# Kernel optimization log

Hardware: AMD Instinct MI355X
Metric: run time of the kernel (lower is better)

The kernel has to match this reference:

```python
import jax, jax.numpy as jnp
import numpy as np

N = 3072        # num_node
R = 7           # num_relation
ATTN_R = 2      # attn_num_relation
SPACE = R - ATTN_R  # space_information_num = 5
D = 64          # hidden dim
H = 4           # num_heads
DH = D // H     # head dim = 16
WINDOW = 128    # window_size
TOPK = 16       # k
TEMP = 0.5      # temperature
EPS = 1e-5
E = N * 16


def _bn(h):
    # BatchNorm1d (training mode, gamma=1, beta=0): normalize over node axis (-2)
    m = h.mean(axis=-2, keepdims=True)
    v = h.var(axis=-2, keepdims=True)
    return (h - m) / jnp.sqrt(v + EPS)


def setup_inputs() -> dict:
    key = jax.random.key(0)
    ks = jax.random.split(key, 12)
    s = 0.1
    return {
        "x": jax.random.normal(ks[0], (N, D), jnp.float32),
        "edge_weight": jnp.ones((E,), jnp.float32),
        "W_rel_s": jax.random.normal(ks[1], (R, D, D), jnp.float32) * s,
        "W_self_s": jax.random.normal(ks[2], (D, D), jnp.float32) * s,
        "b_s": jnp.zeros((D,), jnp.float32),
        "Wq": jax.random.normal(ks[3], (ATTN_R, D, D), jnp.float32) * s,
        "Wk": jax.random.normal(ks[4], (ATTN_R, D, D), jnp.float32) * s,
        "W_msg": jax.random.normal(ks[5], (R * D, D), jnp.float32) * s,
        "W_self_g": jax.random.normal(ks[6], (D, D), jnp.float32) * s,
        "b_g": jnp.zeros((D,), jnp.float32),
        "node_in": jax.random.randint(ks[7], (E,), 0, N, jnp.int32),
        "node_out": jax.random.randint(ks[8], (E,), 0, N, jnp.int32),
        "relation": jax.random.randint(ks[9], (E,), 0, R, jnp.int32),
    }


def reference(x, edge_weight, W_rel_s, W_self_s, b_s, Wq, Wk, W_msg,
              W_self_g, b_g, node_in, node_out, relation):
    # ---- dense adjacency A[r, i, j] = weight of edge (i -> j, relation r) ----
    # equivalent to sparse_coo(...).to_dense().t().view(N,R,N).permute(1,0,2)
    A = jnp.zeros((R, N, N), x.dtype).at[relation, node_in, node_out].add(edge_weight)

    # ---- relationalGraphStack: per-relation conv -> [R, N, D] ----
    msg = jnp.einsum('rij,id->rjd', A, x)                       # aggregate in-neighbors
    rel_out = jax.nn.relu(_bn(jnp.einsum('rjd,rde->rje', msg, W_rel_s)
                              + x @ W_self_s + b_s))            # [R, N, D]

    # ---- Rewirescorelayer on attention relations ----
    attn_in = rel_out[SPACE:]                                   # [ATTN_R, N, D]
    q = jnp.einsum('rnd,rde->rne', attn_in, Wq).reshape(ATTN_R, N, H, DH)
    kk = jnp.einsum('rnd,rde->rne', attn_in, Wk).reshape(ATTN_R, N, H, DH)
    scores = jnp.einsum('rnhd,rmhd->rhnm', q, kk) / np.sqrt(DH).astype(np.float32)
    idx = jnp.arange(N)
    wmask = jnp.abs(idx[:, None] - idx[None, :]) <= WINDOW      # local window
    scores = jnp.where(wmask[None, None], scores, -1e9)
    probs = jax.nn.softmax(scores / TEMP, axis=-1).mean(axis=1)  # [ATTN_R, N, N]
    kth = jax.lax.top_k(probs, TOPK)[0][..., -1:]
    S = jnp.where(probs >= kth, probs, 0.0)                     # hard top-k per row
    attn_output = jnp.transpose(S, (1, 0, 2)).reshape(N, ATTN_R * N)

    # ---- fuse with adjacency: max over attention blocks, keep spatial blocks ----
    adj2d = jnp.transpose(A, (1, 0, 2)).reshape(N, R * N)       # [i, r*N + j]
    attn_output = jnp.maximum(adj2d[:, SPACE * N:], attn_output)
    new_edge_list = jnp.concatenate([attn_output, adj2d[:, :SPACE * N]], axis=1)

    # ---- rewireGearNetstack: GearNet conv with dense rewired adjacency ----
    B = jnp.transpose(new_edge_list.reshape(N, R, N), (1, 0, 2))  # [R, i, j]
    msg2 = jnp.einsum('rij,id->jrd', B, x).reshape(N, R * D)      # [N, R*D]
    hidden = jax.nn.relu(_bn(msg2 @ W_msg + x @ W_self_g + b_g))  # [N, D]

    graph_feature = hidden.sum(axis=0, keepdims=True)             # SumReadout, 1 graph
    return graph_feature, hidden, new_edge_list
```

## Files before the change

### kernel.cpp

```cpp
#include <hip/hip_runtime.h>
#include <cmath>

constexpr int kN    = 3072;
constexpr int kR    = 7;
constexpr int kSPC  = 5;
constexpr int kD    = 64;
constexpr int kWIN  = 128;
constexpr int kTOPK = 16;
constexpr int kE    = kN * 16;
constexpr int kRN   = kR * kN;
constexpr int kRD   = kR * kD;
constexpr float kEPS = 1e-5f;

__device__ __forceinline__ float wred_max(float v) {
#pragma unroll
  for (int off = 32; off; off >>= 1) v = fmaxf(v, __shfl_xor(v, off));
  return v;
}
__device__ __forceinline__ float wred_sum(float v) {
#pragma unroll
  for (int off = 32; off; off >>= 1) v += __shfl_xor(v, off);
  return v;
}

__global__ __launch_bounds__(256) void k_fill0(float4* __restrict__ p, size_t n4) {
  size_t i = (size_t)blockIdx.x * 256 + threadIdx.x;
  const size_t stride = (size_t)gridDim.x * 256;
  const float4 z = make_float4(0.f, 0.f, 0.f, 0.f);
  for (; i < n4; i += stride) p[i] = z;
}

__global__ __launch_bounds__(256) void k_scatter(
    const float* __restrict__ x, const float* __restrict__ ew,
    const int* __restrict__ nin, const int* __restrict__ nout,
    const int* __restrict__ rel,
    float* __restrict__ msg2, float* __restrict__ msgA, float* __restrict__ nel) {
  const int e = blockIdx.x * 4 + (threadIdx.x >> 6);
  const int lane = threadIdx.x & 63;
  const int r = rel[e], i = nin[e], j = nout[e];
  const float w = ew[e];
  const float v = w * x[i * kD + lane];
  if (r < kSPC) {
    atomicAdd(&msg2[(size_t)j * kRD + (r + 2) * kD + lane], v);
    if (lane == 0) atomicAdd(&nel[(size_t)i * kRN + (size_t)(r + 2) * kN + j], w);
  } else {
    const int k = r - kSPC;
    atomicAdd(&msgA[(size_t)(k * kN + j) * kD + lane], v);
    if (lane == 0) atomicAdd(&nel[(size_t)i * kRN + (size_t)k * kN + j], w);
  }
}

__global__ __launch_bounds__(256) void k_h1(
    const float* __restrict__ x, const float* __restrict__ msgA,
    const float* __restrict__ Wrel, const float* __restrict__ Wself,
    const float* __restrict__ bs, float* __restrict__ h1) {
  const int k = blockIdx.y;
  const int e = threadIdx.x & 63;
  const int rl = threadIdx.x >> 6;
  const int n = blockIdx.x * 4 + rl;
  __shared__ float a[4][kD], xx[4][kD];
  a[rl][e] = msgA[(size_t)(k * kN + n) * kD + e];
  xx[rl][e] = x[n * kD + e];
  __syncthreads();
  const float* Wr = Wrel + (size_t)(kSPC + k) * kD * kD;
  float acc = bs[e];
#pragma unroll 8
  for (int d = 0; d < kD; ++d)
    acc += a[rl][d] * Wr[d * kD + e] + xx[rl][d] * Wself[d * kD + e];
  h1[(size_t)(k * kN + n) * kD + e] = acc;
}

__global__ __launch_bounds__(256) void k_bnstats(
    const float* __restrict__ h, float* __restrict__ mean, float* __restrict__ inv) {
  const int c = blockIdx.x;
  const int mat = c >> 6, e = c & 63;
  const float* p = h + (size_t)mat * kN * kD + e;
  float s = 0.f, s2 = 0.f;
  for (int n = threadIdx.x; n < kN; n += 256) {
    float v = p[(size_t)n * kD];
    s += v; s2 += v * v;
  }
  __shared__ float sh0[256], sh1[256];
  sh0[threadIdx.x] = s; sh1[threadIdx.x] = s2;
  __syncthreads();
  for (int off = 128; off > 0; off >>= 1) {
    if (threadIdx.x < off) { sh0[threadIdx.x] += sh0[threadIdx.x + off]; sh1[threadIdx.x] += sh1[threadIdx.x + off]; }
    __syncthreads();
  }
  if (threadIdx.x == 0) {
    float m = sh0[0] / (float)kN;
    float var = sh1[0] / (float)kN - m * m;
    mean[c] = m;
    inv[c] = rsqrtf(var + kEPS);
  }
}

__global__ __launch_bounds__(256) void k_qk(
    const float* __restrict__ h1, const float* __restrict__ mean,
    const float* __restrict__ inv, const float* __restrict__ Wq,
    const float* __restrict__ Wk, float* __restrict__ qb, float* __restrict__ kb) {
  const int k = blockIdx.y;
  const int e = threadIdx.x & 63;
  const int rl = threadIdx.x >> 6;
  const int n = blockIdx.x * 4 + rl;
  __shared__ float a[4][kD];
  float v = h1[(size_t)(k * kN + n) * kD + e];
  v = (v - mean[k * 64 + e]) * inv[k * 64 + e];
  a[rl][e] = v > 0.f ? v : 0.f;
  __syncthreads();
  const float* wq = Wq + (size_t)k * kD * kD;
  const float* wk = Wk + (size_t)k * kD * kD;
  float aq = 0.f, ak = 0.f;
#pragma unroll 8
  for (int d = 0; d < kD; ++d) {
    float av = a[rl][d];
    aq += av * wq[d * kD + e];
    ak += av * wk[d * kD + e];
  }
  qb[(size_t)(k * kN + n) * kD + e] = aq;
  kb[(size_t)(k * kN + n) * kD + e] = ak;
}

__global__ __launch_bounds__(256) void k_attn(
    const float* __restrict__ qb, const float* __restrict__ kb,
    const float* __restrict__ x, float* __restrict__ nel,
    float* __restrict__ msg2, int* __restrict__ selCols, int* __restrict__ selCnt) {
  const int lane = threadIdx.x & 63;
  const int w = threadIdx.x >> 6;
  const int idx = blockIdx.x * 4 + w;
  const int k = idx / kN;
  const int n = idx - k * kN;
  __shared__ float qs[4][kD];
  __shared__ float sval[4][64];
  __shared__ int scol[4][64];
  qs[w][lane] = qb[(size_t)(k * kN + n) * kD + lane];
  __syncthreads();
  const int lo = n - kWIN < 0 ? 0 : n - kWIN;
  const int hi = n + kWIN > kN - 1 ? kN - 1 : n + kWIN;

  float sc[5][4];
#pragma unroll
  for (int s = 0; s < 5; ++s) {
    const int m = lo + s * 64 + lane;
    if (m <= hi) {
      const float4* krow = reinterpret_cast<const float4*>(kb + (size_t)(k * kN + m) * kD);
#pragma unroll
      for (int h = 0; h < 4; ++h) {
        float acc = 0.f;
#pragma unroll
        for (int g = 0; g < 4; ++g) {
          float4 kv = krow[h * 4 + g];
          const float* qp = &qs[w][h * 16 + g * 4];
          acc += kv.x * qp[0] + kv.y * qp[1] + kv.z * qp[2] + kv.w * qp[3];
        }
        sc[s][h] = acc * 0.5f;
      }
    } else {
#pragma unroll
      for (int h = 0; h < 4; ++h) sc[s][h] = -3.0e38f;
    }
  }

  float pm[5] = {0.f, 0.f, 0.f, 0.f, 0.f};
#pragma unroll
  for (int h = 0; h < 4; ++h) {
    float lm = fmaxf(fmaxf(fmaxf(sc[0][h], sc[1][h]), fmaxf(sc[2][h], sc[3][h])), sc[4][h]);
    float mx = wred_max(lm);
    float eh[5], den = 0.f;
#pragma unroll
    for (int s = 0; s < 5; ++s) {
      eh[s] = (sc[s][h] > -1.0e38f) ? expf(sc[s][h] - mx) : 0.f;
      den += eh[s];
    }
    den = wred_sum(den);
    float rdn = 1.f / den;
#pragma unroll
    for (int s = 0; s < 5; ++s) pm[s] += eh[s] * rdn;
  }
#pragma unroll
  for (int s = 0; s < 5; ++s) pm[s] *= 0.25f;

  float rem[5];
#pragma unroll
  for (int s = 0; s < 5; ++s) {
    const int m = lo + s * 64 + lane;
    rem[s] = (m <= hi) ? pm[s] : -1.f;
  }
  float kth = 0.f;
  for (int t = 0; t < kTOPK; ++t) {
    float lm = fmaxf(fmaxf(fmaxf(rem[0], rem[1]), fmaxf(rem[2], rem[3])), rem[4]);
    float gm = wred_max(lm);
    unsigned long long b = __ballot(lm == gm);
    int src = __ffsll((unsigned long long)b) - 1;
    if (lane == src) {
      if (rem[0] == gm) rem[0] = -2.f;
      else if (rem[1] == gm) rem[1] = -2.f;
      else if (rem[2] == gm) rem[2] = -2.f;
      else if (rem[3] == gm) rem[3] = -2.f;
      else rem[4] = -2.f;
    }
    kth = gm;
  }

  bool sel[5];
  int cl = 0;
#pragma unroll
  for (int s = 0; s < 5; ++s) {
    const int m = lo + s * 64 + lane;
    sel[s] = (m <= hi) && (pm[s] >= kth);
    cl += sel[s] ? 1 : 0;
  }
  int v = cl;
#pragma unroll
  for (int off = 1; off < 64; off <<= 1) {
    int t = __shfl_up(v, off);
    if (lane >= off) v += t;
  }
  const int excl = v - cl;
  const int total = __shfl(v, 63);
  const int tot = total < 64 ? total : 64;
  const int rowbase = (k * kN + n) * 64;
  int p = excl;
#pragma unroll
  for (int s = 0; s < 5; ++s) {
    if (sel[s] && p < 64) {
      const int m = lo + s * 64 + lane;
      const size_t cell = (size_t)n * kRN + (size_t)k * kN + m;
      float a = nel[cell];
      float fin = fmaxf(a, pm[s]);
      nel[cell] = fin;
      scol[w][p] = m;
      sval[w][p] = fin;
      selCols[rowbase + p] = m;
      ++p;
    }
  }
  if (lane == 0) selCnt[k * kN + n] = tot;

  const float xv = x[n * kD + lane];
  for (int t = 0; t < tot; ++t) {
    const int m = scol[w][t];
    const float fv = sval[w][t];
    atomicAdd(&msg2[(size_t)m * kRD + k * kD + lane], fv * xv);
  }
}

__global__ __launch_bounds__(256) void k_edgefix(
    const float* __restrict__ x, const float* __restrict__ ew,
    const int* __restrict__ nin, const int* __restrict__ nout,
    const int* __restrict__ rel, const int* __restrict__ selCols,
    const int* __restrict__ selCnt, float* __restrict__ msg2) {
  const int e = blockIdx.x * 4 + (threadIdx.x >> 6);
  const int lane = threadIdx.x & 63;
  const int r = rel[e];
  if (r < kSPC) return;
  const int k = r - kSPC, i = nin[e], j = nout[e];
  int diff = i - j; if (diff < 0) diff = -diff;
  if (diff <= kWIN) {
    const int cnt = selCnt[k * kN + i];
    bool mine = (lane < cnt) && (selCols[(k * kN + i) * 64 + lane] == j);
    if (__ballot(mine)) return;
  }
  atomicAdd(&msg2[(size_t)j * kRD + k * kD + lane], ew[e] * x[i * kD + lane]);
}

__global__ __launch_bounds__(256) void k_hpre(
    const float* __restrict__ msg2, const float* __restrict__ x,
    const float* __restrict__ Wmsg, const float* __restrict__ Wg,
    const float* __restrict__ bg, float* __restrict__ hpre) {
  const int e = threadIdx.x & 63;
  const int rl = threadIdx.x >> 6;
  const int n0 = blockIdx.x * 4;
  __shared__ float ml[4][kRD];
  __shared__ float xl[4][kD];
  for (int idx = threadIdx.x; idx < 4 * kRD; idx += 256) {
    int rr = idx / kRD, c = idx - rr * kRD;
    ml[rr][c] = msg2[(size_t)(n0 + rr) * kRD + c];
  }
  {
    int rr = threadIdx.x >> 6, c = threadIdx.x & 63;
    xl[rr][c] = x[(n0 + rr) * kD + c];
  }
  __syncthreads();
  float acc = bg[e];
#pragma unroll 8
  for (int c = 0; c < kRD; ++c) acc += ml[rl][c] * Wmsg[c * kD + e];
#pragma unroll 8
  for (int d = 0; d < kD; ++d) acc += xl[rl][d] * Wg[d * kD + e];
  hpre[(size_t)(n0 + rl) * kD + e] = acc;
}

__global__ __launch_bounds__(256) void k_hfin(
    float* __restrict__ hid, const float* __restrict__ mean,
    const float* __restrict__ inv, float* __restrict__ gf) {
  const int e = threadIdx.x & 63;
  const int rl = threadIdx.x >> 6;
  const int n = blockIdx.x * 4 + rl;
  float v = hid[(size_t)n * kD + e];
  v = (v - mean[e]) * inv[e];
  v = v > 0.f ? v : 0.f;
  hid[(size_t)n * kD + e] = v;
  __shared__ float sh[4][kD];
  sh[rl][e] = v;
  __syncthreads();
  if (threadIdx.x < 64)
    atomicAdd(&gf[e], sh[0][e] + sh[1][e] + sh[2][e] + sh[3][e]);
}

extern "C" void kernel_launch(void* const* d_in, const int* in_sizes, int n_in,
                              void* d_out, int out_size, void* d_ws, size_t ws_size,
                              hipStream_t stream) {
  (void)in_sizes; (void)n_in; (void)ws_size;
  const float* x     = (const float*)d_in[0];
  const float* ew    = (const float*)d_in[1];
  const float* Wrel  = (const float*)d_in[2];
  const float* Wself = (const float*)d_in[3];
  const float* bs    = (const float*)d_in[4];
  const float* Wq    = (const float*)d_in[5];
  const float* Wk    = (const float*)d_in[6];
  const float* Wmsg  = (const float*)d_in[7];
  const float* Wg    = (const float*)d_in[8];
  const float* bg    = (const float*)d_in[9];
  const int*   nin   = (const int*)d_in[10];
  const int*   nout  = (const int*)d_in[11];
  const int*   rel   = (const int*)d_in[12];

  float* gf  = (float*)d_out;
  float* hid = gf + 64;
  float* nel = hid + (size_t)kN * kD;

  float* w0    = (float*)d_ws;
  float* msg2  = w0;
  float* msgA  = msg2 + (size_t)kN * kRD;
  float* h1    = msgA + (size_t)2 * kN * kD;
  float* qb    = h1   + (size_t)2 * kN * kD;
  float* kb    = qb   + (size_t)2 * kN * kD;
  float* mean1 = kb   + (size_t)2 * kN * kD;
  float* inv1  = mean1 + 128;
  float* mean2 = inv1 + 128;
  float* inv2  = mean2 + 64;
  int* selCols = (int*)(inv2 + 64);
  int* selCnt  = selCols + (size_t)2 * kN * 64;

  k_fill0<<<2048, 256, 0, stream>>>((float4*)d_out, (size_t)out_size / 4);
  k_fill0<<<512, 256, 0, stream>>>((float4*)msg2,
                                   (size_t)(kN * kRD + 2 * kN * kD) / 4);

  k_scatter<<<kE / 4, 256, 0, stream>>>(x, ew, nin, nout, rel, msg2, msgA, nel);
  dim3 g2(kN / 4, 2);
  k_h1<<<g2, 256, 0, stream>>>(x, msgA, Wrel, Wself, bs, h1);
  k_bnstats<<<128, 256, 0, stream>>>(h1, mean1, inv1);
  k_qk<<<g2, 256, 0, stream>>>(h1, mean1, inv1, Wq, Wk, qb, kb);
  k_attn<<<(2 * kN) / 4, 256, 0, stream>>>(qb, kb, x, nel, msg2, selCols, selCnt);
  k_edgefix<<<kE / 4, 256, 0, stream>>>(x, ew, nin, nout, rel, selCols, selCnt, msg2);
  k_hpre<<<kN / 4, 256, 0, stream>>>(msg2, x, Wmsg, Wg, bg, hid);
  k_bnstats<<<64, 256, 0, stream>>>(hid, mean2, inv2);
  k_hfin<<<kN / 4, 256, 0, stream>>>(hid, mean2, inv2, gf);
}
```

Before: 228.2 us.

## Spread dense edge-list zero-fill across pipeline kernels and write it last

The large dense new_edge_list output (about 264 MB) is no longer zeroed up front in one fill kernel. Its zeroing is split into eight chunks, and each chunk is cleared inside one of the existing compute kernels. Edge weights for the attention relations inside the window now go into a compact windowed buffer that the attention kernel reads. The final dense cells are written at the end by two small scatter kernels, one for the edges and one for the selected top-k values. This is meant to overlap the memory-bound fill with latency-bound compute, at the cost of extra grid-stride loops in every kernel and more workspace.

Measured after the change: 223.8 us. No clear change (-1.9%).

```diff
diff --git a/kernel.cpp b/kernel.cpp
--- a/kernel.cpp
+++ b/kernel.cpp
@@ -10,7 +10,13 @@
 constexpr int kE    = kN * 16;
 constexpr int kRN   = kR * kN;
 constexpr int kRD   = kR * kD;
+constexpr int kAW   = 2 * kWIN + 1;
 constexpr float kEPS = 1e-5f;
+
+constexpr size_t kNelF = (size_t)kN * kRN;
+constexpr size_t kNelQ = kNelF / 4;
+constexpr int    kCar  = 8;
+constexpr size_t kChunkQ = kNelQ / kCar;
 
 __device__ __forceinline__ float wred_max(float v) {
 #pragma unroll
@@ -23,18 +29,31 @@
   return v;
 }
 
-__global__ __launch_bounds__(256) void k_fill0(float4* __restrict__ p, size_t n4) {
+__device__ __forceinline__ void fill_chunk(float4* __restrict__ nel4, int cid) {
+  const size_t beg = (size_t)cid * kChunkQ;
+  const size_t end = beg + kChunkQ;
+  const size_t nth = (size_t)gridDim.x * gridDim.y * blockDim.x;
+  size_t tid = ((size_t)blockIdx.y * gridDim.x + blockIdx.x) * blockDim.x + threadIdx.x;
+  const float4 z = make_float4(0.f, 0.f, 0.f, 0.f);
+  for (size_t i = beg + tid; i < end; i += nth) nel4[i] = z;
+}
+
+__global__ __launch_bounds__(256) void k_fill_ws(float4* __restrict__ p, size_t n4,
+                                                 float* __restrict__ gf) {
   size_t i = (size_t)blockIdx.x * 256 + threadIdx.x;
   const size_t stride = (size_t)gridDim.x * 256;
   const float4 z = make_float4(0.f, 0.f, 0.f, 0.f);
   for (; i < n4; i += stride) p[i] = z;
-}
-
-__global__ __launch_bounds__(256) void k_scatter(
+  if (blockIdx.x == 0 && threadIdx.x < 64) gf[threadIdx.x] = 0.f;
+}
+
+__global__ __launch_bounds__(256) void k_scatter_msg(
     const float* __restrict__ x, const float* __restrict__ ew,
     const int* __restrict__ nin, const int* __restrict__ nout,
-    const int* __restrict__ rel,
-    float* __restrict__ msg2, float* __restrict__ msgA, float* __restrict__ nel) {
+    const int* __restrict__ rel, float* __restrict__ msg2,
+    float* __restrict__ msgA, float* __restrict__ awin,
+    float4* __restrict__ nel4) {
+  fill_chunk(nel4, 0);
   const int e = blockIdx.x * 4 + (threadIdx.x >> 6);
   const int lane = threadIdx.x & 63;
   const int r = rel[e], i = nin[e], j = nout[e];
@@ -42,18 +61,21 @@
   const float v = w * x[i * kD + lane];
   if (r < kSPC) {
     atomicAdd(&msg2[(size_t)j * kRD + (r + 2) * kD + lane], v);
-    if (lane == 0) atomicAdd(&nel[(size_t)i * kRN + (size_t)(r + 2) * kN + j], w);
   } else {
     const int k = r - kSPC;
     atomicAdd(&msgA[(size_t)(k * kN + j) * kD + lane], v);
-    if (lane == 0) atomicAdd(&nel[(size_t)i * kRN + (size_t)k * kN + j], w);
+    const int diff = j - i;
+    if (lane == 0 && diff >= -kWIN && diff <= kWIN)
+      atomicAdd(&awin[(size_t)(k * kN + i) * kAW + (diff + kWIN)], w);
   }
 }
 
 __global__ __launch_bounds__(256) void k_h1(
     const float* __restrict__ x, const float* __restrict__ msgA,
     const float* __restrict__ Wrel, const float* __restrict__ Wself,
-    const float* __restrict__ bs, float* __restrict__ h1) {
+    const float* __restrict__ bs, float* __restrict__ h1,
+    float4* __restrict__ nel4) {
+  fill_chunk(nel4, 1);
   const int k = blockIdx.y;
   const int e = threadIdx.x & 63;
   const int rl = threadIdx.x >> 6;
@@ -71,7 +93,9 @@
 }
 
 __global__ __launch_bounds__(256) void k_bnstats(
-    const float* __restrict__ h, float* __restrict__ mean, float* __restrict__ inv) {
+    const float* __restrict__ h, float* __restrict__ mean, float* __restrict__ inv,
+    float4* __restrict__ nel4, int cid) {
+  fill_chunk(nel4, cid);
   const int c = blockIdx.x;
   const int mat = c >> 6, e = c & 63;
   const float* p = h + (size_t)mat * kN * kD + e;
@@ -98,7 +122,9 @@
 __global__ __launch_bounds__(256) void k_qk(
     const float* __restrict__ h1, const float* __restrict__ mean,
     const float* __restrict__ inv, const float* __restrict__ Wq,
-    const float* __restrict__ Wk, float* __restrict__ qb, float* __restrict__ kb) {
+    const float* __restrict__ Wk, float* __restrict__ qb, float* __restrict__ kb,
+    float4* __restrict__ nel4) {
+  fill_chunk(nel4, 3);
   const int k = blockIdx.y;
   const int e = threadIdx.x & 63;
   const int rl = threadIdx.x >> 6;
@@ -123,8 +149,10 @@
 
 __global__ __launch_bounds__(256) void k_attn(
     const float* __restrict__ qb, const float* __restrict__ kb,
-    const float* __restrict__ x, float* __restrict__ nel,
-    float* __restrict__ msg2, int* __restrict__ selCols, int* __restrict__ selCnt) {
+    const float* __restrict__ x, const float* __restrict__ awin,
+    float* __restrict__ msg2, int* __restrict__ selCols,
+    float* __restrict__ selVals, int* __restrict__ selCnt,
+    float4* __restrict__ nel4) {
   const int lane = threadIdx.x & 63;
   const int w = threadIdx.x >> 6;
   const int idx = blockIdx.x * 4 + w;
@@ -219,23 +247,22 @@
   const int excl = v - cl;
   const int total = __shfl(v, 63);
   const int tot = total < 64 ? total : 64;
-  const int rowbase = (k * kN + n) * 64;
+  const int rowbase = idx * 64;
   int p = excl;
 #pragma unroll
   for (int s = 0; s < 5; ++s) {
     if (sel[s] && p < 64) {
       const int m = lo + s * 64 + lane;
-      const size_t cell = (size_t)n * kRN + (size_t)k * kN + m;
-      float a = nel[cell];
-      float fin = fmaxf(a, pm[s]);
-      nel[cell] = fin;
+      const float a = awin[(size_t)idx * kAW + (m - n + kWIN)];
+      const float fin = fmaxf(a, pm[s]);
       scol[w][p] = m;
       sval[w][p] = fin;
       selCols[rowbase + p] = m;
+      selVals[rowbase + p] = fin;
       ++p;
     }
   }
-  if (lane == 0) selCnt[k * kN + n] = tot;
+  if (lane == 0) selCnt[idx] = tot;
 
   const float xv = x[n * kD + lane];
   for (int t = 0; t < tot; ++t) {
@@ -243,13 +270,16 @@
     const float fv = sval[w][t];
     atomicAdd(&msg2[(size_t)m * kRD + k * kD + lane], fv * xv);
   }
+  fill_chunk(nel4, 4);
 }
 
 __global__ __launch_bounds__(256) void k_edgefix(
     const float* __restrict__ x, const float* __restrict__ ew,
     const int* __restrict__ nin, const int* __restrict__ nout,
     const int* __restrict__ rel, const int* __restrict__ selCols,
-    const int* __restrict__ selCnt, float* __restrict__ msg2) {
+    const int* __restrict__ selCnt, float* __restrict__ msg2,
+    float4* __restrict__ nel4) {
+  fill_chunk(nel4, 5);
   const int e = blockIdx.x * 4 + (threadIdx.x >> 6);
   const int lane = threadIdx.x & 63;
   const int r = rel[e];
@@ -267,7 +297,9 @@
 __global__ __launch_bounds__(256) void k_hpre(
     const float* __restrict__ msg2, const float* __restrict__ x,
     const float* __restrict__ Wmsg, const float* __restrict__ Wg,
-    const float* __restrict__ bg, float* __restrict__ hpre) {
+    const float* __restrict__ bg, float* __restrict__ hpre,
+    float4* __restrict__ nel4) {
+  fill_chunk(nel4, 6);
   const int e = threadIdx.x & 63;
   const int rl = threadIdx.x >> 6;
   const int n0 = blockIdx.x * 4;
@@ -288,6 +320,30 @@
 #pragma unroll 8
   for (int d = 0; d < kD; ++d) acc += xl[rl][d] * Wg[d * kD + e];
   hpre[(size_t)(n0 + rl) * kD + e] = acc;
+}
+
+__global__ __launch_bounds__(256) void k_nel_edges(
+    const float* __restrict__ ew, const int* __restrict__ nin,
+    const int* __restrict__ nout, const int* __restrict__ rel,
+    float* __restrict__ nel) {
+  const int e = blockIdx.x * 256 + threadIdx.x;
+  if (e >= kE) return;
+  const int r = rel[e], i = nin[e], j = nout[e];
+  const int col = (r < kSPC) ? (r + 2) * kN + j : (r - kSPC) * kN + j;
+  atomicAdd(&nel[(size_t)i * kRN + col], ew[e]);
+}
+
+__global__ __launch_bounds__(256) void k_nel_sel(
+    const int* __restrict__ selCols, const float* __restrict__ selVals,
+    const int* __restrict__ selCnt, float* __restrict__ nel) {
+  const int idx = blockIdx.x * 4 + (threadIdx.x >> 6);
+  const int lane = threadIdx.x & 63;
+  const int k = idx / kN, n = idx - k * kN;
+  const int cnt = selCnt[idx];
+  if (lane < cnt) {
+    const int m = selCols[idx * 64 + lane];
+    nel[(size_t)n * kRN + (size_t)k * kN + m] = selVals[idx * 64 + lane];
+  }
 }
 
 __global__ __launch_bounds__(256) void k_hfin(
@@ -310,7 +366,7 @@
 extern "C" void kernel_launch(void* const* d_in, const int* in_sizes, int n_in,
                               void* d_out, int out_size, void* d_ws, size_t ws_size,
                               hipStream_t stream) {
-  (void)in_sizes; (void)n_in; (void)ws_size;
+  (void)in_sizes; (void)n_in; (void)ws_size; (void)out_size;
   const float* x     = (const float*)d_in[0];
   const float* ew    = (const float*)d_in[1];
   const float* Wrel  = (const float*)d_in[2];
@@ -328,32 +384,36 @@
   float* gf  = (float*)d_out;
   float* hid = gf + 64;
   float* nel = hid + (size_t)kN * kD;
-
-  float* w0    = (float*)d_ws;
-  float* msg2  = w0;
-  float* msgA  = msg2 + (size_t)kN * kRD;
-  float* h1    = msgA + (size_t)2 * kN * kD;
-  float* qb    = h1   + (size_t)2 * kN * kD;
-  float* kb    = qb   + (size_t)2 * kN * kD;
-  float* mean1 = kb   + (size_t)2 * kN * kD;
-  float* inv1  = mean1 + 128;
-  float* mean2 = inv1 + 128;
-  float* inv2  = mean2 + 64;
-  int* selCols = (int*)(inv2 + 64);
-  int* selCnt  = selCols + (size_t)2 * kN * 64;
-
-  k_fill0<<<2048, 256, 0, stream>>>((float4*)d_out, (size_t)out_size / 4);
-  k_fill0<<<512, 256, 0, stream>>>((float4*)msg2,
-                                   (size_t)(kN * kRD + 2 * kN * kD) / 4);
-
-  k_scatter<<<kE / 4, 256, 0, stream>>>(x, ew, nin, nout, rel, msg2, msgA, nel);
+  float4* nel4 = (float4*)nel;
+
+  float* w0     = (float*)d_ws;
+  float* msg2   = w0;
+  float* msgA   = msg2 + (size_t)kN * kRD;
+  float* awin   = msgA + (size_t)2 * kN * kD;
+  float* h1     = awin + (size_t)2 * kN * kAW;
+  float* qb     = h1   + (size_t)2 * kN * kD;
+  float* kb     = qb   + (size_t)2 * kN * kD;
+  float* mean1  = kb   + (size_t)2 * kN * kD;
+  float* inv1   = mean1 + 128;
+  float* mean2  = inv1 + 128;
+  float* inv2   = mean2 + 64;
+  float* selVals= inv2 + 64;
+  int* selCols  = (int*)(selVals + (size_t)2 * kN * 64);
+  int* selCnt   = selCols + (size_t)2 * kN * 64;
+
+  const size_t wsZeroF = (size_t)kN * kRD + (size_t)2 * kN * kD + (size_t)2 * kN * kAW;
+
+  k_fill_ws<<<1024, 256, 0, stream>>>((float4*)w0, wsZeroF / 4, gf);
+  k_scatter_msg<<<kE / 4, 256, 0, stream>>>(x, ew, nin, nout, rel, msg2, msgA, awin, nel4);
   dim3 g2(kN / 4, 2);
-  k_h1<<<g2, 256, 0, stream>>>(x, msgA, Wrel, Wself, bs, h1);
-  k_bnstats<<<128, 256, 0, stream>>>(h1, mean1, inv1);
-  k_qk<<<g2, 256, 0, stream>>>(h1, mean1, inv1, Wq, Wk, qb, kb);
-  k_attn<<<(2 * kN) / 4, 256, 0, stream>>>(qb, kb, x, nel, msg2, selCols, selCnt);
-  k_edgefix<<<kE / 4, 256, 0, stream>>>(x, ew, nin, nout, rel, selCols, selCnt, msg2);
-  k_hpre<<<kN / 4, 256, 0, stream>>>(msg2, x, Wmsg, Wg, bg, hid);
-  k_bnstats<<<64, 256, 0, stream>>>(hid, mean2, inv2);
+  k_h1<<<g2, 256, 0, stream>>>(x, msgA, Wrel, Wself, bs, h1, nel4);
+  k_bnstats<<<128, 256, 0, stream>>>(h1, mean1, inv1, nel4, 2);
+  k_qk<<<g2, 256, 0, stream>>>(h1, mean1, inv1, Wq, Wk, qb, kb, nel4);
+  k_attn<<<(2 * kN) / 4, 256, 0, stream>>>(qb, kb, x, awin, msg2, selCols, selVals, selCnt, nel4);
+  k_edgefix<<<kE / 4, 256, 0, stream>>>(x, ew, nin, nout, rel, selCols, selCnt, msg2, nel4);
+  k_hpre<<<kN / 4, 256, 0, stream>>>(msg2, x, Wmsg, Wg, bg, hid, nel4);
+  k_bnstats<<<64, 256, 0, stream>>>(hid, mean2, inv2, nel4, 7);
+  k_nel_edges<<<(kE + 255) / 256, 256, 0, stream>>>(ew, nin, nout, rel, nel);
+  k_nel_sel<<<(2 * kN) / 4, 256, 0, stream>>>(selCols, selVals, selCnt, nel);
   k_hfin<<<kN / 4, 256, 0, stream>>>(hid, mean2, inv2, gf);
 }
```
